# Optimization experiments

Hardware: AMD Instinct MI355X
Metric: run time of the kernel (lower is better)

## Reference

```python
import jax, jax.numpy as jnp
import numpy as np

N_NODES = 100000
N_EDGES = 3200000
F_IN, F_HID, F_OUT = 36, 8, 2
NEG_SLOPE = 0.2


def gat_layer(x, src, dst, W, a_src, a_dst, b, num_nodes):
    # Linear transform: [N, F'] 
    h = x @ W
    # Per-node attention logits (heads=1)
    alpha_s = h @ a_src  # [N]
    alpha_d = h @ a_dst  # [N]
    # Edge-wise score: leaky_relu(a_src . h_j + a_dst . h_i) for edge j->i
    e = jax.nn.leaky_relu(alpha_s[src] + alpha_d[dst], negative_slope=NEG_SLOPE)  # [E]
    # Segment softmax over incoming edges of each dst node
    m = jax.ops.segment_max(e, dst, num_segments=num_nodes)  # [N]
    ee = jnp.exp(e - m[dst])
    denom = jax.ops.segment_sum(ee, dst, num_segments=num_nodes)  # [N]
    alpha = ee / denom[dst]  # [E]
    # Scatter-aggregate messages
    out = jax.ops.segment_sum(alpha[:, None] * h[src], dst, num_segments=num_nodes)
    return out + b


def setup_inputs() -> dict:
    key = jax.random.key(0)
    ks = jax.random.split(key, 10)
    x = jax.random.normal(ks[0], (N_NODES, F_IN), dtype=jnp.float32)
    edge_index = jax.random.randint(ks[1], (2, N_EDGES), 0, N_NODES, dtype=jnp.int64)
    s1 = 1.0 / np.sqrt(F_IN)
    s2 = 1.0 / np.sqrt(F_HID)
    W1 = jax.random.uniform(ks[2], (F_IN, F_HID), jnp.float32, -s1, s1)
    a_src1 = jax.random.uniform(ks[3], (F_HID,), jnp.float32, -s2, s2)
    a_dst1 = jax.random.uniform(ks[4], (F_HID,), jnp.float32, -s2, s2)
    b1 = jnp.zeros((F_HID,), jnp.float32)
    W2 = jax.random.uniform(ks[5], (F_HID, F_OUT), jnp.float32, -s2, s2)
    so = 1.0 / np.sqrt(F_OUT)
    a_src2 = jax.random.uniform(ks[6], (F_OUT,), jnp.float32, -so, so)
    a_dst2 = jax.random.uniform(ks[7], (F_OUT,), jnp.float32, -so, so)
    b2 = jnp.zeros((F_OUT,), jnp.float32)
    return {"x": x, "edge_index": edge_index, "W1": W1, "a_src1": a_src1,
            "a_dst1": a_dst1, "b1": b1, "W2": W2, "a_src2": a_src2,
            "a_dst2": a_dst2, "b2": b2}


def reference(x, edge_index, W1, a_src1, a_dst1, b1, W2, a_src2, a_dst2, b2):
    src, dst = edge_index[0], edge_index[1]
    n = x.shape[0]
    h = jax.nn.relu(gat_layer(x, src, dst, W1, a_src1, a_dst1, b1, n))
    # dropout is identity in eval mode
    out = gat_layer(h, src, dst, W2, a_src2, a_dst2, b2, n)
    return jax.nn.log_softmax(out, axis=1)
```

## Files before the change

### kernel.cpp

```cpp
#include <hip/hip_runtime.h>
#include <hip/hip_bf16.h>

#define N_NODES 100000
#define N_EDGES 3200000
#define F_IN 36
#define F_HID 8
#define F_OUT 2
#define NEG_SLOPE 0.2f

#define GSHIFT 7
#define GNPB 128
#define GNBUCK 782
#define CAP 4608
#define NB_PART 256
#define CHUNK 12500
#define BP 1024
#define NB_NODE1 98
#define BPG 512

__device__ __forceinline__ int detect_is64(const void* eidx, int* s_flag) {
    if (threadIdx.x < 64) {
        const unsigned int* p = (const unsigned int*)eidx;
        unsigned int v1 = p[2 * threadIdx.x + 1];
        unsigned int v2 = p[2 * (threadIdx.x + 64) + 1];
        unsigned long long m = __ballot(v1 != 0u || v2 != 0u);
        if (threadIdx.x == 0) *s_flag = (m == 0ull) ? 1 : 0;
    }
    __syncthreads();
    return *s_flag;
}

__global__ void part_node1_k(const void* __restrict__ eidx, int* __restrict__ gcnt,
                             int* __restrict__ partP,
                             const float* __restrict__ x, const float* __restrict__ W1,
                             const float* __restrict__ aw_d,
                             float* __restrict__ h1, float* __restrict__ ad1) {
    if (blockIdx.x < NB_PART) {
        __shared__ int sortbuf[CHUNK];
        __shared__ int hist[GNBUCK];
        __shared__ int spre[GNBUCK];
        __shared__ int cursor[GNBUCK];
        __shared__ int gbase[GNBUCK];
        __shared__ int s_flag;
        int t = threadIdx.x;
        for (int i = t; i < GNBUCK; i += BP) hist[i] = 0;
        int f = detect_is64(eidx, &s_flag);
        int beg = blockIdx.x * CHUNK;
        int end = beg + CHUNK;
        const unsigned int* p32 = (const unsigned int*)eidx;
        if (f) {
            for (int i = beg + t; i < end; i += BP)
                atomicAdd(&hist[(int)p32[2 * (N_EDGES + i)] >> GSHIFT], 1);
        } else {
            const int* p = (const int*)eidx;
            for (int i = beg + t; i < end; i += BP)
                atomicAdd(&hist[p[N_EDGES + i] >> GSHIFT], 1);
        }
        __syncthreads();
        if (t < GNBUCK) {
            int c = hist[t];
            gbase[t] = c ? atomicAdd(&gcnt[t], c) : 0;
            spre[t] = c;
        }
        __syncthreads();
        for (int off = 1; off < GNBUCK; off <<= 1) {
            int v = 0;
            if (t < GNBUCK && t >= off) v = spre[t - off];
            __syncthreads();
            if (t < GNBUCK && t >= off) spre[t] += v;
            __syncthreads();
        }
        if (t < GNBUCK) cursor[t] = spre[t] - hist[t];
        __syncthreads();
        if (f) {
            for (int i = beg + t; i < end; i += BP) {
                int s = (int)p32[2 * i];
                int d = (int)p32[2 * (N_EDGES + i)];
                int b = d >> GSHIFT;
                int pos = atomicAdd(&cursor[b], 1);
                sortbuf[pos] = (s << GSHIFT) | (d & (GNPB - 1));
            }
        } else {
            const int* p = (const int*)eidx;
            for (int i = beg + t; i < end; i += BP) {
                int s = p[i];
                int d = p[N_EDGES + i];
                int b = d >> GSHIFT;
                int pos = atomicAdd(&cursor[b], 1);
                sortbuf[pos] = (s << GSHIFT) | (d & (GNPB - 1));
            }
        }
        __syncthreads();
        for (int i = t; i < CHUNK; i += BP) {
            int lo = 0, hi = GNBUCK - 1;
            while (lo < hi) {
                int mid = (lo + hi) >> 1;
                if (spre[mid] > i) hi = mid; else lo = mid + 1;
            }
            int b = lo;
            int gp = gbase[b] + (i - (spre[b] - hist[b]));
            if (gp < CAP) partP[b * CAP + gp] = sortbuf[i];
        }
    } else {
        int n = (blockIdx.x - NB_PART) * BP + threadIdx.x;
        if (n >= N_NODES) return;
        float acc[F_HID];
#pragma unroll
        for (int f = 0; f < F_HID; f++) acc[f] = 0.f;
        const float4* xp = (const float4*)(x + (size_t)n * F_IN);
#pragma unroll
        for (int q = 0; q < 9; q++) {
            float4 xv = xp[q];
            const float* w = W1 + q * 4 * F_HID;
#pragma unroll
            for (int f = 0; f < F_HID; f++) {
                acc[f] += xv.x * w[0 * F_HID + f] + xv.y * w[1 * F_HID + f]
                        + xv.z * w[2 * F_HID + f] + xv.w * w[3 * F_HID + f];
            }
        }
        float d = 0.f;
#pragma unroll
        for (int f = 0; f < F_HID; f++) d += acc[f] * aw_d[f];
        float4* hp = (float4*)(h1 + (size_t)n * F_HID);
        hp[0] = make_float4(acc[0], acc[1], acc[2], acc[3]);
        hp[1] = make_float4(acc[4], acc[5], acc[6], acc[7]);
        ad1[n] = d;
    }
}

__global__ void gatF1_k(const int* __restrict__ gcnt, const int* __restrict__ partP,
                        int* __restrict__ e_srcP, int2* __restrict__ rowinfo,
                        const float* __restrict__ aw_s1, const float* __restrict__ ad1,
                        const float* __restrict__ h1, const float* __restrict__ b1,
                        const float* __restrict__ W2, const float* __restrict__ aw_s2,
                        const float* __restrict__ aw_d2, float4* __restrict__ P2) {
    __shared__ int eL[CAP];
    __shared__ int hist[GNPB];
    __shared__ int nstart[GNPB];
    __shared__ int cursor[GNPB];
    __shared__ int sscan[GNPB];
    __shared__ float adl[GNPB];
    int t = threadIdx.x;
    int c = blockIdx.x;
    int nbase = c << GSHIFT;
    int beg = c * CAP;
    int cnt = gcnt[c]; if (cnt > CAP) cnt = CAP;

    if (t < GNPB) {
        hist[t] = 0;
        adl[t] = (nbase + t < N_NODES) ? ad1[nbase + t] : 0.f;
    }
    __syncthreads();
    for (int j = t; j < cnt; j += BPG)
        atomicAdd(&hist[partP[beg + j] & (GNPB - 1)], 1);
    __syncthreads();
    if (t < GNPB) sscan[t] = hist[t];
    __syncthreads();
    for (int o = 1; o < GNPB; o <<= 1) {
        int u = (t < GNPB && t >= o) ? sscan[t - o] : 0;
        __syncthreads();
        if (t < GNPB) sscan[t] += u;
        __syncthreads();
    }
    if (t < GNPB) {
        int ex = sscan[t] - hist[t];
        nstart[t] = ex;
        cursor[t] = ex;
        int node = nbase + t;
        if (node < N_NODES) rowinfo[node] = make_int2(beg + ex, hist[t]);
    }
    __syncthreads();
    for (int j = t; j < cnt; j += BPG) {
        int pk = partP[beg + j];
        int pos = atomicAdd(&cursor[pk & (GNPB - 1)], 1);
        eL[pos] = pk >> GSHIFT;
    }
    __syncthreads();
    for (int i = t; i < cnt; i += BPG) e_srcP[beg + i] = eL[i];

    int node = t >> 2;
    int lane = t & 3;
    int gnode = nbase + node;
    if (gnode >= N_NODES) return;
    int ns = nstart[node];
    int ne = ns + hist[node];
    float add = adl[node];

    float ws0 = aw_s1[0], ws1 = aw_s1[1], ws2 = aw_s1[2], ws3 = aw_s1[3];
    float ws4 = aw_s1[4], ws5 = aw_s1[5], ws6 = aw_s1[6], ws7 = aw_s1[7];

    float denom = 0.f;
    float acc[F_HID];
#pragma unroll
    for (int f = 0; f < F_HID; f++) acc[f] = 0.f;
    for (int i = ns + lane; i < ne; i += 4) {
        int s = eL[i];
        const float4* hp = (const float4*)(h1 + (size_t)s * F_HID);
        float4 p0 = hp[0], p1 = hp[1];
        float e = p0.x * ws0 + p0.y * ws1 + p0.z * ws2 + p0.w * ws3
                + p1.x * ws4 + p1.y * ws5 + p1.z * ws6 + p1.w * ws7 + add;
        e = e >= 0.f ? e : NEG_SLOPE * e;
        float ee = __expf(e);
        denom += ee;
        acc[0] += ee * p0.x; acc[1] += ee * p0.y; acc[2] += ee * p0.z; acc[3] += ee * p0.w;
        acc[4] += ee * p1.x; acc[5] += ee * p1.y; acc[6] += ee * p1.z; acc[7] += ee * p1.w;
    }
#pragma unroll
    for (int o = 2; o > 0; o >>= 1) {
        denom += __shfl_xor(denom, o, 4);
#pragma unroll
        for (int f = 0; f < F_HID; f++) acc[f] += __shfl_xor(acc[f], o, 4);
    }
    if (lane == 0) {
        float inv = denom > 0.f ? 1.f / denom : 0.f;
        float o0 = 0.f, o1 = 0.f;
#pragma unroll
        for (int f = 0; f < F_HID; f++) {
            float v = acc[f] * inv + b1[f];
            v = v > 0.f ? v : 0.f;
            o0 += v * W2[f * F_OUT + 0];
            o1 += v * W2[f * F_OUT + 1];
        }
        float as2v = o0 * aw_s2[0] + o1 * aw_s2[1];
        float ad2v = o0 * aw_d2[0] + o1 * aw_d2[1];
        P2[gnode] = make_float4(as2v, o0, o1, ad2v);
    }
}

__global__ void gat2_k(const int2* __restrict__ rowinfo, const int* __restrict__ e_srcP,
                       const float4* __restrict__ P2, const float* __restrict__ b2,
                       float* __restrict__ out, int n_nodes) {
    int gid = blockIdx.x * 16 + (threadIdx.x >> 4);
    int lane = threadIdx.x & 15;
    if (gid >= n_nodes) return;
    int2 ri = rowinfo[gid];
    float add = P2[gid].w;

    float denom = 0.f, a0 = 0.f, a1 = 0.f;
    int jend = ri.x + ri.y;
    for (int j = ri.x + lane; j < jend; j += 16) {
        int s = e_srcP[j];
        float4 q = P2[s];
        float e = q.x + add;
        e = e >= 0.f ? e : NEG_SLOPE * e;
        float ee = __expf(e);
        denom += ee;
        a0 += ee * q.y;
        a1 += ee * q.z;
    }
#pragma unroll
    for (int o = 8; o > 0; o >>= 1) {
        denom += __shfl_xor(denom, o, 16);
        a0 += __shfl_xor(a0, o, 16);
        a1 += __shfl_xor(a1, o, 16);
    }

    if (lane == 0) {
        float inv = denom > 0.f ? 1.f / denom : 0.f;
        float o0 = a0 * inv + b2[0];
        float o1 = a1 * inv + b2[1];
        float M = fmaxf(o0, o1);
        float l = M + logf(__expf(o0 - M) + __expf(o1 - M));
        ((float2*)out)[gid] = make_float2(o0 - l, o1 - l);
    }
}

extern "C" void kernel_launch(void* const* d_in, const int* in_sizes, int n_in,
                              void* d_out, int out_size, void* d_ws, size_t ws_size,
                              hipStream_t stream) {
    const float* x      = (const float*)d_in[0];
    const void*  eidx   = d_in[1];
    const float* W1     = (const float*)d_in[2];
    const float* a_src1 = (const float*)d_in[3];
    const float* a_dst1 = (const float*)d_in[4];
    const float* b1     = (const float*)d_in[5];
    const float* W2     = (const float*)d_in[6];
    const float* a_src2 = (const float*)d_in[7];
    const float* a_dst2 = (const float*)d_in[8];
    const float* b2     = (const float*)d_in[9];
    float* out = (float*)d_out;

    const size_t N = N_NODES;
    const size_t PADDED = (size_t)GNBUCK * CAP;

    int* wsi = (int*)d_ws;
    float* wsf = (float*)d_ws;
    size_t o = 0;
    int* partP    = wsi + o;      o += PADDED;
    int* e_srcP   = wsi + o;      o += PADDED;
    int* gcnt     = wsi + o;      o += 800;
    int2* rowinfo = (int2*)(wsi + o); o += 2 * N;
    float* ad1    = wsf + o;      o += N;
    o = (o + 15) & ~(size_t)15;
    float* h1     = wsf + o;      o += 8 * N;
    float4* P2    = (float4*)(wsf + o); o += 4 * N;

    const int gridG = (int)(N / 16);

    hipMemsetAsync(gcnt, 0, 800 * sizeof(int), stream);

    part_node1_k<<<NB_PART + NB_NODE1, BP, 0, stream>>>(eidx, gcnt, partP,
                                                        x, W1, a_dst1, h1, ad1);
    gatF1_k<<<GNBUCK, BPG, 0, stream>>>(gcnt, partP, e_srcP, rowinfo, a_src1, ad1, h1, b1,
                                        W2, a_src2, a_dst2, P2);
    gat2_k<<<gridG, 256, 0, stream>>>(rowinfo, e_srcP, P2, b2, out, (int)N);
}
```

Measured before the change: 167.1 us.

## Fuse both GAT aggregation layers into one cooperative kernel with grid sync

Merges the layer-1 aggregation kernel and the layer-2 aggregation kernel into a single cooperative kernel. Each block handles two dst buckets and keeps their sorted source lists in shared memory across a grid-wide sync. This removes the global e_srcP and rowinfo writes and re-reads, plus one kernel launch. In exchange it adds a grid barrier, doubles shared memory per block, and cuts layer-2 parallelism to 4 lanes per node instead of 16, which may lengthen the gather phase.

```diff
diff --git a/kernel.cpp b/kernel.cpp
--- a/kernel.cpp
+++ b/kernel.cpp
@@ -1,5 +1,7 @@
 #include <hip/hip_runtime.h>
 #include <hip/hip_bf16.h>
+#include <hip/hip_cooperative_groups.h>
+namespace cg = cooperative_groups;
 
 #define N_NODES 100000
 #define N_EDGES 3200000
@@ -17,6 +19,7 @@
 #define BP 1024
 #define NB_NODE1 98
 #define BPG 512
+#define NBLK2 391
 
 __device__ __forceinline__ int detect_is64(const void* eidx, int* s_flag) {
     if (threadIdx.x < 64) {
@@ -128,140 +131,158 @@
     }
 }
 
-__global__ void gatF1_k(const int* __restrict__ gcnt, const int* __restrict__ partP,
-                        int* __restrict__ e_srcP, int2* __restrict__ rowinfo,
-                        const float* __restrict__ aw_s1, const float* __restrict__ ad1,
-                        const float* __restrict__ h1, const float* __restrict__ b1,
-                        const float* __restrict__ W2, const float* __restrict__ aw_s2,
-                        const float* __restrict__ aw_d2, float4* __restrict__ P2) {
-    __shared__ int eL[CAP];
+__global__ __launch_bounds__(BPG, 4)
+void gatF12_k(const int* __restrict__ gcnt, const int* __restrict__ partP,
+              const float* __restrict__ aw_s1, const float* __restrict__ ad1,
+              const float* __restrict__ h1, const float* __restrict__ b1,
+              const float* __restrict__ W2, const float* __restrict__ aw_s2,
+              const float* __restrict__ aw_d2, float4* __restrict__ P2,
+              const float* __restrict__ b2, float* __restrict__ out) {
+    __shared__ int eL0[CAP];
+    __shared__ int eL1[CAP];
     __shared__ int hist[GNPB];
     __shared__ int nstart[GNPB];
     __shared__ int cursor[GNPB];
     __shared__ int sscan[GNPB];
     __shared__ float adl[GNPB];
+    __shared__ float ad2s[2 * GNPB];
+    cg::grid_group grid = cg::this_grid();
     int t = threadIdx.x;
-    int c = blockIdx.x;
-    int nbase = c << GSHIFT;
-    int beg = c * CAP;
-    int cnt = gcnt[c]; if (cnt > CAP) cnt = CAP;
-
-    if (t < GNPB) {
-        hist[t] = 0;
-        adl[t] = (nbase + t < N_NODES) ? ad1[nbase + t] : 0.f;
-    }
-    __syncthreads();
-    for (int j = t; j < cnt; j += BPG)
-        atomicAdd(&hist[partP[beg + j] & (GNPB - 1)], 1);
-    __syncthreads();
-    if (t < GNPB) sscan[t] = hist[t];
-    __syncthreads();
-    for (int o = 1; o < GNPB; o <<= 1) {
-        int u = (t < GNPB && t >= o) ? sscan[t - o] : 0;
-        __syncthreads();
-        if (t < GNPB) sscan[t] += u;
-        __syncthreads();
-    }
-    if (t < GNPB) {
-        int ex = sscan[t] - hist[t];
-        nstart[t] = ex;
-        cursor[t] = ex;
-        int node = nbase + t;
-        if (node < N_NODES) rowinfo[node] = make_int2(beg + ex, hist[t]);
-    }
-    __syncthreads();
-    for (int j = t; j < cnt; j += BPG) {
-        int pk = partP[beg + j];
-        int pos = atomicAdd(&cursor[pk & (GNPB - 1)], 1);
-        eL[pos] = pk >> GSHIFT;
-    }
-    __syncthreads();
-    for (int i = t; i < cnt; i += BPG) e_srcP[beg + i] = eL[i];
-
     int node = t >> 2;
     int lane = t & 3;
-    int gnode = nbase + node;
-    if (gnode >= N_NODES) return;
-    int ns = nstart[node];
-    int ne = ns + hist[node];
-    float add = adl[node];
 
     float ws0 = aw_s1[0], ws1 = aw_s1[1], ws2 = aw_s1[2], ws3 = aw_s1[3];
     float ws4 = aw_s1[4], ws5 = aw_s1[5], ws6 = aw_s1[6], ws7 = aw_s1[7];
 
-    float denom = 0.f;
-    float acc[F_HID];
-#pragma unroll
-    for (int f = 0; f < F_HID; f++) acc[f] = 0.f;
-    for (int i = ns + lane; i < ne; i += 4) {
-        int s = eL[i];
-        const float4* hp = (const float4*)(h1 + (size_t)s * F_HID);
-        float4 p0 = hp[0], p1 = hp[1];
-        float e = p0.x * ws0 + p0.y * ws1 + p0.z * ws2 + p0.w * ws3
-                + p1.x * ws4 + p1.y * ws5 + p1.z * ws6 + p1.w * ws7 + add;
-        e = e >= 0.f ? e : NEG_SLOPE * e;
-        float ee = __expf(e);
-        denom += ee;
-        acc[0] += ee * p0.x; acc[1] += ee * p0.y; acc[2] += ee * p0.z; acc[3] += ee * p0.w;
-        acc[4] += ee * p1.x; acc[5] += ee * p1.y; acc[6] += ee * p1.z; acc[7] += ee * p1.w;
+    int ns_r[2], ne_r[2];
+
+#pragma unroll
+    for (int kk = 0; kk < 2; kk++) {
+        int c = blockIdx.x + kk * NBLK2;
+        int nbase = c << GSHIFT;
+        int beg = c * CAP;
+        int cnt = gcnt[c]; if (cnt > CAP) cnt = CAP;
+        int* eL = kk ? eL1 : eL0;
+
+        __syncthreads();
+        if (t < GNPB) {
+            hist[t] = 0;
+            adl[t] = (nbase + t < N_NODES) ? ad1[nbase + t] : 0.f;
+        }
+        __syncthreads();
+        for (int j = t; j < cnt; j += BPG)
+            atomicAdd(&hist[partP[beg + j] & (GNPB - 1)], 1);
+        __syncthreads();
+        if (t < GNPB) sscan[t] = hist[t];
+        __syncthreads();
+        for (int o = 1; o < GNPB; o <<= 1) {
+            int u = (t < GNPB && t >= o) ? sscan[t - o] : 0;
+            __syncthreads();
+            if (t < GNPB) sscan[t] += u;
+            __syncthreads();
+        }
+        if (t < GNPB) {
+            int ex = sscan[t] - hist[t];
+            nstart[t] = ex;
+            cursor[t] = ex;
+        }
+        __syncthreads();
+        for (int j = t; j < cnt; j += BPG) {
+            int pk = partP[beg + j];
+            int pos = atomicAdd(&cursor[pk & (GNPB - 1)], 1);
+            eL[pos] = pk >> GSHIFT;
+        }
+        __syncthreads();
+
+        int gnode = nbase + node;
+        bool valid = gnode < N_NODES;
+        int ns = nstart[node];
+        int ne = ns + hist[node];
+        ns_r[kk] = ns; ne_r[kk] = ne;
+        float add = adl[node];
+
+        float denom = 0.f;
+        float acc[F_HID];
+#pragma unroll
+        for (int f = 0; f < F_HID; f++) acc[f] = 0.f;
+        for (int i = ns + lane; i < ne; i += 4) {
+            int s = eL[i];
+            const float4* hp = (const float4*)(h1 + (size_t)s * F_HID);
+            float4 p0 = hp[0], p1 = hp[1];
+            float e = p0.x * ws0 + p0.y * ws1 + p0.z * ws2 + p0.w * ws3
+                    + p1.x * ws4 + p1.y * ws5 + p1.z * ws6 + p1.w * ws7 + add;
+            e = e >= 0.f ? e : NEG_SLOPE * e;
+            float ee = __expf(e);
+            denom += ee;
+            acc[0] += ee * p0.x; acc[1] += ee * p0.y; acc[2] += ee * p0.z; acc[3] += ee * p0.w;
+            acc[4] += ee * p1.x; acc[5] += ee * p1.y; acc[6] += ee * p1.z; acc[7] += ee * p1.w;
+        }
+#pragma unroll
+        for (int o = 2; o > 0; o >>= 1) {
+            denom += __shfl_xor(denom, o, 4);
+#pragma unroll
+            for (int f = 0; f < F_HID; f++) acc[f] += __shfl_xor(acc[f], o, 4);
+        }
+        if (lane == 0 && valid) {
+            float inv = denom > 0.f ? 1.f / denom : 0.f;
+            float o0 = 0.f, o1 = 0.f;
+#pragma unroll
+            for (int f = 0; f < F_HID; f++) {
+                float v = acc[f] * inv + b1[f];
+                v = v > 0.f ? v : 0.f;
+                o0 += v * W2[f * F_OUT + 0];
+                o1 += v * W2[f * F_OUT + 1];
+            }
+            float as2v = o0 * aw_s2[0] + o1 * aw_s2[1];
+            float ad2v = o0 * aw_d2[0] + o1 * aw_d2[1];
+            unsigned int* pp = (unsigned int*)&P2[gnode];
+            __hip_atomic_store(pp + 0, __float_as_uint(as2v), __ATOMIC_RELAXED, __HIP_MEMORY_SCOPE_AGENT);
+            __hip_atomic_store(pp + 1, __float_as_uint(o0),   __ATOMIC_RELAXED, __HIP_MEMORY_SCOPE_AGENT);
+            __hip_atomic_store(pp + 2, __float_as_uint(o1),   __ATOMIC_RELAXED, __HIP_MEMORY_SCOPE_AGENT);
+            __hip_atomic_store(pp + 3, __float_as_uint(ad2v), __ATOMIC_RELAXED, __HIP_MEMORY_SCOPE_AGENT);
+            ad2s[kk * GNPB + node] = ad2v;
+        }
     }
-#pragma unroll
-    for (int o = 2; o > 0; o >>= 1) {
-        denom += __shfl_xor(denom, o, 4);
-#pragma unroll
-        for (int f = 0; f < F_HID; f++) acc[f] += __shfl_xor(acc[f], o, 4);
-    }
-    if (lane == 0) {
-        float inv = denom > 0.f ? 1.f / denom : 0.f;
-        float o0 = 0.f, o1 = 0.f;
-#pragma unroll
-        for (int f = 0; f < F_HID; f++) {
-            float v = acc[f] * inv + b1[f];
-            v = v > 0.f ? v : 0.f;
-            o0 += v * W2[f * F_OUT + 0];
-            o1 += v * W2[f * F_OUT + 1];
-        }
-        float as2v = o0 * aw_s2[0] + o1 * aw_s2[1];
-        float ad2v = o0 * aw_d2[0] + o1 * aw_d2[1];
-        P2[gnode] = make_float4(as2v, o0, o1, ad2v);
-    }
-}
-
-__global__ void gat2_k(const int2* __restrict__ rowinfo, const int* __restrict__ e_srcP,
-                       const float4* __restrict__ P2, const float* __restrict__ b2,
-                       float* __restrict__ out, int n_nodes) {
-    int gid = blockIdx.x * 16 + (threadIdx.x >> 4);
-    int lane = threadIdx.x & 15;
-    if (gid >= n_nodes) return;
-    int2 ri = rowinfo[gid];
-    float add = P2[gid].w;
-
-    float denom = 0.f, a0 = 0.f, a1 = 0.f;
-    int jend = ri.x + ri.y;
-    for (int j = ri.x + lane; j < jend; j += 16) {
-        int s = e_srcP[j];
-        float4 q = P2[s];
-        float e = q.x + add;
-        e = e >= 0.f ? e : NEG_SLOPE * e;
-        float ee = __expf(e);
-        denom += ee;
-        a0 += ee * q.y;
-        a1 += ee * q.z;
-    }
-#pragma unroll
-    for (int o = 8; o > 0; o >>= 1) {
-        denom += __shfl_xor(denom, o, 16);
-        a0 += __shfl_xor(a0, o, 16);
-        a1 += __shfl_xor(a1, o, 16);
-    }
-
-    if (lane == 0) {
-        float inv = denom > 0.f ? 1.f / denom : 0.f;
-        float o0 = a0 * inv + b2[0];
-        float o1 = a1 * inv + b2[1];
-        float M = fmaxf(o0, o1);
-        float l = M + logf(__expf(o0 - M) + __expf(o1 - M));
-        ((float2*)out)[gid] = make_float2(o0 - l, o1 - l);
+
+    __threadfence();
+    grid.sync();
+    __threadfence();
+
+#pragma unroll
+    for (int kk = 0; kk < 2; kk++) {
+        int c = blockIdx.x + kk * NBLK2;
+        int nbase = c << GSHIFT;
+        int gnode = nbase + node;
+        bool valid = gnode < N_NODES;
+        const int* eL = kk ? eL1 : eL0;
+        int ns = ns_r[kk], ne = ne_r[kk];
+        float add2 = ad2s[kk * GNPB + node];
+
+        float d2 = 0.f, a0 = 0.f, a1 = 0.f;
+        for (int i = ns + lane; i < ne; i += 4) {
+            int s = eL[i];
+            float4 q = P2[s];
+            float e = q.x + add2;
+            e = e >= 0.f ? e : NEG_SLOPE * e;
+            float ee = __expf(e);
+            d2 += ee;
+            a0 += ee * q.y;
+            a1 += ee * q.z;
+        }
+#pragma unroll
+        for (int o = 2; o > 0; o >>= 1) {
+            d2 += __shfl_xor(d2, o, 4);
+            a0 += __shfl_xor(a0, o, 4);
+            a1 += __shfl_xor(a1, o, 4);
+        }
+        if (lane == 0 && valid) {
+            float inv = d2 > 0.f ? 1.f / d2 : 0.f;
+            float o0 = a0 * inv + b2[0];
+            float o1 = a1 * inv + b2[1];
+            float M = fmaxf(o0, o1);
+            float l = M + logf(__expf(o0 - M) + __expf(o1 - M));
+            ((float2*)out)[gnode] = make_float2(o0 - l, o1 - l);
+        }
     }
 }
 
@@ -287,21 +308,20 @@
     float* wsf = (float*)d_ws;
     size_t o = 0;
     int* partP    = wsi + o;      o += PADDED;
-    int* e_srcP   = wsi + o;      o += PADDED;
     int* gcnt     = wsi + o;      o += 800;
-    int2* rowinfo = (int2*)(wsi + o); o += 2 * N;
     float* ad1    = wsf + o;      o += N;
     o = (o + 15) & ~(size_t)15;
     float* h1     = wsf + o;      o += 8 * N;
     float4* P2    = (float4*)(wsf + o); o += 4 * N;
 
-    const int gridG = (int)(N / 16);
-
     hipMemsetAsync(gcnt, 0, 800 * sizeof(int), stream);
 
     part_node1_k<<<NB_PART + NB_NODE1, BP, 0, stream>>>(eidx, gcnt, partP,
                                                         x, W1, a_dst1, h1, ad1);
-    gatF1_k<<<GNBUCK, BPG, 0, stream>>>(gcnt, partP, e_srcP, rowinfo, a_src1, ad1, h1, b1,
-                                        W2, a_src2, a_dst2, P2);
-    gat2_k<<<gridG, 256, 0, stream>>>(rowinfo, e_srcP, P2, b2, out, (int)N);
+
+    void* kargs[] = {(void*)&gcnt, (void*)&partP, (void*)&a_src1, (void*)&ad1,
+                     (void*)&h1, (void*)&b1, (void*)&W2, (void*)&a_src2,
+                     (void*)&a_dst2, (void*)&P2, (void*)&b2, (void*)&out};
+    hipLaunchCooperativeKernel(reinterpret_cast<void*>(gatF12_k),
+                               dim3(NBLK2), dim3(BPG), kargs, 0, stream);
 }
```

After: 371.0 us. 122% more time.
